# Kernel optimization log

Measured on AMD Instinct MI355X. Metric: run time of the kernel, lower is better.

## Reference

```python
import jax, jax.numpy as jnp
import numpy as np

N = 100_000      # nodes
E = 1_600_000    # edges (avg degree 16)
F = 64           # node feature dim (node_channels)
H = 64           # hidden_channels
ED = 16          # edge_embedding_size
NEG_SLOPE = 0.2


def _lin(k, fi, fo):
    return jax.random.normal(k, (fi, fo), jnp.float32) / np.sqrt(fi)


def setup_inputs() -> dict:
    key = jax.random.key(0)
    ks = jax.random.split(key, 24)
    inp = {
        "x": jax.random.normal(ks[0], (N, F), jnp.float32),
        "edge_index": jax.random.randint(ks[1], (2, E), 0, N, dtype=jnp.int64),
        "edge_attr": jax.random.normal(ks[2], (E, ED), jnp.float32),
        # conv1 (GATv2Conv -> H)
        "Wl1": _lin(ks[3], F, H), "bl1": jnp.zeros((H,), jnp.float32),
        "Wr1": _lin(ks[4], F, H), "br1": jnp.zeros((H,), jnp.float32),
        "We1": _lin(ks[5], ED, H),
        "a1": jax.random.normal(ks[6], (H,), jnp.float32) / np.sqrt(H),
        "cb1": jnp.zeros((H,), jnp.float32),
        # lin1 residual (F -> H)
        "L1w": _lin(ks[7], F, H), "L1b": jnp.zeros((H,), jnp.float32),
        # conv2 (GATv2Conv -> F)
        "Wl2": _lin(ks[8], H, F), "bl2": jnp.zeros((F,), jnp.float32),
        "Wr2": _lin(ks[9], H, F), "br2": jnp.zeros((F,), jnp.float32),
        "We2": _lin(ks[10], ED, F),
        "a2": jax.random.normal(ks[11], (F,), jnp.float32) / np.sqrt(F),
        "cb2": jnp.zeros((F,), jnp.float32),
        # lin2 residual (H -> F)
        "L2w": _lin(ks[12], H, F), "L2b": jnp.zeros((F,), jnp.float32),
    }
    return inp


def _gatv2(x, src, dst, edge_attr, Wl, bl, Wr, br, We, a, cb):
    # GATv2, heads=1, add_self_loops=False, lin_edge bias-free
    xl = x @ Wl + bl                      # [N, D] source transform (also the value)
    xr = x @ Wr + br                      # [N, D] target transform
    m = xl[src] + xr[dst] + edge_attr @ We  # [E, D]
    s = jax.nn.leaky_relu(m, NEG_SLOPE) @ a  # [E] attention logits
    smax = jax.ops.segment_max(s, dst, num_segments=N)
    ex = jnp.exp(s - smax[dst])
    den = jax.ops.segment_sum(ex, dst, num_segments=N)
    alpha = ex / (den[dst] + 1e-16)       # softmax over incoming edges per target
    out = jax.ops.segment_sum(alpha[:, None] * xl[src], dst, num_segments=N)
    return out + cb


def reference(x, edge_index, edge_attr,
              Wl1, bl1, Wr1, br1, We1, a1, cb1, L1w, L1b,
              Wl2, bl2, Wr2, br2, We2, a2, cb2, L2w, L2b):
    src, dst = edge_index[0], edge_index[1]
    h = _gatv2(x, src, dst, edge_attr, Wl1, bl1, Wr1, br1, We1, a1, cb1) + x @ L1w + L1b
    h = jax.nn.relu(h)
    out = _gatv2(h, src, dst, edge_attr, Wl2, bl2, Wr2, br2, We2, a2, cb2) + h @ L2w + L2b
    return out
```

## Files before the change

### kernel.cpp

```cpp
#include <hip/hip_runtime.h>
#include <hip/hip_fp16.h>
#include <math.h>

#define D 64
#define EDIM 16
#define NEG 0.2f
#define SCHUNK 1024

typedef _Float16 hh2 __attribute__((ext_vector_type(2)));
union H2cvt { unsigned u; hh2 v; __half2 h; };

__global__ void node_transform(const float* __restrict__ x,
                               const float* __restrict__ Wl, const float* __restrict__ bl,
                               const float* __restrict__ Wr, const float* __restrict__ br,
                               const float* __restrict__ Lw, const float* __restrict__ Lb,
                               __half* __restrict__ xlh, float* __restrict__ xr,
                               float* __restrict__ res, int N)
{
    __shared__ float wl[D * D], wr[D * D], lw[D * D];
    for (int i = threadIdx.x; i < D * D / 4; i += blockDim.x) {
        ((float4*)wl)[i] = ((const float4*)Wl)[i];
        ((float4*)wr)[i] = ((const float4*)Wr)[i];
        ((float4*)lw)[i] = ((const float4*)Lw)[i];
    }
    int lane = threadIdx.x & 63;
    int wave = __builtin_amdgcn_readfirstlane(threadIdx.x >> 6);
    float vbl = bl[lane], vbr = br[lane], vlb = Lb[lane];
    __syncthreads();

    int gwave  = blockIdx.x * 4 + wave;
    int nwaves = gridDim.x * 4;
    for (int n0 = gwave * 8; n0 < N; n0 += nwaves * 8) {
        float al[8], ar[8], ae[8];
        #pragma unroll
        for (int j = 0; j < 8; j++) { al[j] = vbl; ar[j] = vbr; ae[j] = vlb; }

        if (n0 + 8 <= N) {
            const float* xp0 = x + (size_t)n0 * D;
            #pragma unroll 4
            for (int k = 0; k < D; k++) {
                float w1 = wl[k * D + lane];
                float w2 = wr[k * D + lane];
                float w3 = lw[k * D + lane];
                #pragma unroll
                for (int j = 0; j < 8; j++) {
                    float xv = xp0[j * D + k];
                    al[j] = fmaf(xv, w1, al[j]);
                    ar[j] = fmaf(xv, w2, ar[j]);
                    ae[j] = fmaf(xv, w3, ae[j]);
                }
            }
            #pragma unroll
            for (int j = 0; j < 8; j++) {
                int n = n0 + j;
                xlh[(size_t)n * D + lane] = __float2half(al[j]);
                xr[(size_t)n * D + lane]  = ar[j];
                res[(size_t)n * D + lane] = ae[j];
            }
        } else {
            int nr = N - n0;
            for (int k = 0; k < D; k++) {
                float w1 = wl[k * D + lane];
                float w2 = wr[k * D + lane];
                float w3 = lw[k * D + lane];
                for (int j = 0; j < nr; j++) {
                    float xv = x[(size_t)(n0 + j) * D + k];
                    al[j] = fmaf(xv, w1, al[j]);
                    ar[j] = fmaf(xv, w2, ar[j]);
                    ae[j] = fmaf(xv, w3, ae[j]);
                }
            }
            for (int j = 0; j < nr; j++) {
                int n = n0 + j;
                xlh[(size_t)n * D + lane] = __float2half(al[j]);
                xr[(size_t)n * D + lane]  = ar[j];
                res[(size_t)n * D + lane] = ae[j];
            }
        }
    }
}

__global__ void count_deg(const int* __restrict__ ei, int* __restrict__ deg, int E)
{
    int e = blockIdx.x * blockDim.x + threadIdx.x;
    if (e < E) atomicAdd(&deg[ei[E + e]], 1);
}

__global__ void scan_blocks(const int* __restrict__ deg, int* __restrict__ rowptr,
                            int* __restrict__ bsum, int N)
{
    __shared__ int tsum[256];
    int t = threadIdx.x;
    int base = blockIdx.x * SCHUNK + t * 4;
    int v0 = 0, v1 = 0, v2 = 0, v3 = 0;
    if (base + 3 < N) {
        const int4 q = *(const int4*)(deg + base);
        v0 = q.x; v1 = q.y; v2 = q.z; v3 = q.w;
    } else {
        if (base + 0 < N) v0 = deg[base + 0];
        if (base + 1 < N) v1 = deg[base + 1];
        if (base + 2 < N) v2 = deg[base + 2];
        if (base + 3 < N) v3 = deg[base + 3];
    }
    int local = v0 + v1 + v2 + v3;
    tsum[t] = local;
    __syncthreads();
    for (int off = 1; off < 256; off <<= 1) {
        int x = (t >= off) ? tsum[t - off] : 0;
        __syncthreads();
        tsum[t] += x;
        __syncthreads();
    }
    int excl = tsum[t] - local;
    if (base + 0 < N) rowptr[base + 0] = excl;
    if (base + 1 < N) rowptr[base + 1] = excl + v0;
    if (base + 2 < N) rowptr[base + 2] = excl + v0 + v1;
    if (base + 3 < N) rowptr[base + 3] = excl + v0 + v1 + v2;
    if (t == 0) bsum[blockIdx.x] = tsum[255];
}

__global__ void scan_bsums(int* __restrict__ bsum, int nb, int* __restrict__ rowptrN)
{
    __shared__ int part[256];
    int t = threadIdx.x;
    int C = (nb + 255) / 256;
    int b = t * C, e = min(b + C, nb);
    int sum = 0;
    for (int i = b; i < e; i++) sum += bsum[i];
    part[t] = sum;
    __syncthreads();
    for (int off = 1; off < 256; off <<= 1) {
        int x = (t >= off) ? part[t - off] : 0;
        __syncthreads();
        part[t] += x;
        __syncthreads();
    }
    int running = part[t] - sum;
    for (int i = b; i < e; i++) {
        int v = bsum[i];
        bsum[i] = running;
        running += v;
    }
    if (t == 255) *rowptrN = part[255];
}

__global__ void add_offsets(int* __restrict__ rowptr, const int* __restrict__ bsum, int N)
{
    int i = blockIdx.x * blockDim.x + threadIdx.x;
    if (i < N) rowptr[i] += bsum[i >> 10];
}

__global__ void scatter_edges(const int* __restrict__ ei, const float* __restrict__ eattr,
                              int* __restrict__ cursor,
                              int* __restrict__ esrc, __half* __restrict__ eah, int E)
{
    int e = blockIdx.x * blockDim.x + threadIdx.x;
    if (e >= E) return;
    int dst = ei[E + e];
    int pos = atomicAdd(&cursor[dst], 1);
    esrc[pos] = ei[e];
    const float4* s4 = (const float4*)(eattr + (size_t)e * EDIM);
    float4 f0 = s4[0], f1 = s4[1], f2 = s4[2], f3 = s4[3];
    union { __half2 h[8]; uint4 q[2]; } u;
    u.h[0] = __floats2half2_rn(f0.x, f0.y); u.h[1] = __floats2half2_rn(f0.z, f0.w);
    u.h[2] = __floats2half2_rn(f1.x, f1.y); u.h[3] = __floats2half2_rn(f1.z, f1.w);
    u.h[4] = __floats2half2_rn(f2.x, f2.y); u.h[5] = __floats2half2_rn(f2.z, f2.w);
    u.h[6] = __floats2half2_rn(f3.x, f3.y); u.h[7] = __floats2half2_rn(f3.z, f3.w);
    uint4* d4 = (uint4*)(eah + (size_t)pos * EDIM);
    d4[0] = u.q[0];
    d4[1] = u.q[1];
}

__device__ __forceinline__ float bpx(float v, int addr)
{
    return __int_as_float(__builtin_amdgcn_ds_bpermute(addr, __float_as_int(v)));
}

__device__ __forceinline__ float edge_dot(const __half* __restrict__ eah, int ee,
                                          const hh2* w2)
{
    const unsigned* ea = (const unsigned*)(eah + (size_t)ee * EDIM);
    float acc = 0.f;
    #pragma unroll
    for (int k = 0; k < 8; k++) {
        H2cvt c; c.u = ea[k];
#if defined(__has_builtin) && __has_builtin(__builtin_amdgcn_fdot2)
        acc = __builtin_amdgcn_fdot2(c.v, w2[k], acc, false);
#else
        acc += (float)(c.v[0] * w2[k][0]) + (float)(c.v[1] * w2[k][1]);
#endif
    }
    return acc;
}

__global__ void gat_fused(const int* __restrict__ rowptr, const int* __restrict__ esrc,
                          const __half* __restrict__ eah,
                          const float* __restrict__ We, const float* __restrict__ avec,
                          const __half* __restrict__ xlh, const float* __restrict__ xr,
                          const float* __restrict__ res, const float* __restrict__ cb,
                          float* __restrict__ out, int N, int do_relu)
{
    int wid = __builtin_amdgcn_readfirstlane(
        (int)((blockIdx.x * blockDim.x + threadIdx.x) >> 6));
    int lane = threadIdx.x & 63;
    if (wid >= N) return;

    hh2 w2[8];
    #pragma unroll
    for (int j = 0; j < 8; j++) {
        H2cvt c;
        c.h = __floats2half2_rn(We[(2 * j) * D + lane], We[(2 * j + 1) * D + lane]);
        w2[j] = c.v;
    }
    float av  = avec[lane];
    float xrv = xr[(size_t)wid * D + lane];
    int beg = __builtin_amdgcn_readfirstlane(rowptr[wid]);
    int end = __builtin_amdgcn_readfirstlane(rowptr[wid + 1]);

    const int la4 = lane << 2;
    const int A1 = la4 ^ 4,  A2 = la4 ^ 8,   A3 = la4 ^ 12;
    const int A4 = la4 ^ 16, A8 = la4 ^ 32,  A16 = la4 ^ 64, A32 = la4 ^ 128;

    float S4 = 0.f, Sr = 0.f, O = 0.f;
    int e = beg;
    for (; e + 4 <= end; e += 4) {
        float pp[4], xlv[4];
        #pragma unroll
        for (int j = 0; j < 4; j++) {
            int s = __builtin_amdgcn_readfirstlane(esrc[e + j]);
            xlv[j] = __half2float(xlh[(size_t)s * D + lane]);
            float ew = edge_dot(eah, e + j, w2);
            float m = xlv[j] + xrv + ew;
            float lr = fmaf(NEG, fminf(m, 0.f), fmaxf(m, 0.f));
            pp[j] = lr * av;
        }
        #pragma unroll
        for (int j = 0; j < 4; j++) pp[j] += bpx(pp[j], A1);
        #pragma unroll
        for (int j = 0; j < 4; j++) pp[j] += bpx(pp[j], A2);
        int c0 = lane & 1, c1 = lane & 2;
        float t0 = c0 ? pp[1] : pp[0];
        float t1 = c0 ? pp[3] : pp[2];
        float v  = c1 ? t1 : t0;
        v += bpx(v, A4); v += bpx(v, A8); v += bpx(v, A16); v += bpx(v, A32);
        float ev = __expf(v);
        S4 += ev;
        float q1 = bpx(ev, A1);
        float q2 = bpx(ev, A2);
        float q3 = bpx(ev, A3);
        float y0a = c0 ? xlv[1] : xlv[0], y0b = c0 ? xlv[3] : xlv[2];
        float y1a = c0 ? xlv[0] : xlv[1], y1b = c0 ? xlv[2] : xlv[3];
        float x_c  = c1 ? y0b : y0a;
        float x_c1 = c1 ? y1b : y1a;
        float x_c2 = c1 ? y0a : y0b;
        float x_c3 = c1 ? y1a : y1b;
        O = fmaf(ev, x_c, fmaf(q1, x_c1, fmaf(q2, x_c2, fmaf(q3, x_c3, O))));
    }
    for (; e < end; ++e) {
        int s = __builtin_amdgcn_readfirstlane(esrc[e]);
        float xlv = __half2float(xlh[(size_t)s * D + lane]);
        float ew = edge_dot(eah, e, w2);
        float m = xlv + xrv + ew;
        float lr = fmaf(NEG, fminf(m, 0.f), fmaxf(m, 0.f));
        float p = lr * av;
        p += bpx(p, A1); p += bpx(p, A2); p += bpx(p, A4);
        p += bpx(p, A8); p += bpx(p, A16); p += bpx(p, A32);
        float w = __expf(p);
        Sr += w;
        O = fmaf(w, xlv, O);
    }
    S4 += bpx(S4, A1);
    S4 += bpx(S4, A2);
    float S = S4 + Sr;

    float v = O / (S + 1e-16f) + cb[lane] + res[(size_t)wid * D + lane];
    if (do_relu) v = fmaxf(v, 0.f);
    out[(size_t)wid * D + lane] = v;
}

extern "C" void kernel_launch(void* const* d_in, const int* in_sizes, int n_in,
                              void* d_out, int out_size, void* d_ws, size_t ws_size,
                              hipStream_t stream)
{
    const float* x     = (const float*)d_in[0];
    const int*   ei    = (const int*)d_in[1];
    const float* eattr = (const float*)d_in[2];
    const float* Wl1 = (const float*)d_in[3];  const float* bl1 = (const float*)d_in[4];
    const float* Wr1 = (const float*)d_in[5];  const float* br1 = (const float*)d_in[6];
    const float* We1 = (const float*)d_in[7];  const float* a1  = (const float*)d_in[8];
    const float* cb1 = (const float*)d_in[9];
    const float* L1w = (const float*)d_in[10]; const float* L1b = (const float*)d_in[11];
    const float* Wl2 = (const float*)d_in[12]; const float* bl2 = (const float*)d_in[13];
    const float* Wr2 = (const float*)d_in[14]; const float* br2 = (const float*)d_in[15];
    const float* We2 = (const float*)d_in[16]; const float* a2  = (const float*)d_in[17];
    const float* cb2 = (const float*)d_in[18];
    const float* L2w = (const float*)d_in[19]; const float* L2b = (const float*)d_in[20];

    const int N = in_sizes[0] / D;
    const int E = in_sizes[1] / 2;
    const int NB = (N + SCHUNK - 1) / SCHUNK;

    char* wsb = (char*)d_ws;
    float*  xr   = (float*)wsb;  wsb += (size_t)N * D * sizeof(float);
    float*  res  = (float*)wsb;  wsb += (size_t)N * D * sizeof(float);
    __half* xlh  = (__half*)wsb; wsb += (size_t)N * D * sizeof(__half);
    __half* eah  = (__half*)wsb; wsb += (size_t)E * EDIM * sizeof(__half);
    int* esrc    = (int*)wsb;    wsb += (size_t)E * sizeof(int);
    int* deg     = (int*)wsb;    wsb += (size_t)N * sizeof(int);
    int* rowptr  = (int*)wsb;    wsb += (size_t)(N + 1) * sizeof(int);
    int* cursor  = (int*)wsb;    wsb += (size_t)N * sizeof(int);
    int* bsum    = (int*)wsb;    wsb += (size_t)NB * sizeof(int);

    float* out = (float*)d_out;

    const int et = (E + 255) / 256;
    const int nb = (N + 3) / 4;

    hipMemsetAsync(deg, 0, (size_t)N * sizeof(int), stream);
    count_deg<<<et, 256, 0, stream>>>(ei, deg, E);
    scan_blocks<<<NB, 256, 0, stream>>>(deg, rowptr, bsum, N);
    scan_bsums<<<1, 256, 0, stream>>>(bsum, NB, rowptr + N);
    add_offsets<<<(N + 255) / 256, 256, 0, stream>>>(rowptr, bsum, N);
    hipMemcpyAsync(cursor, rowptr, (size_t)N * sizeof(int),
                   hipMemcpyDeviceToDevice, stream);
    scatter_edges<<<et, 256, 0, stream>>>(ei, eattr, cursor, esrc, eah, E);

    node_transform<<<1024, 256, 0, stream>>>(x, Wl1, bl1, Wr1, br1, L1w, L1b,
                                             xlh, xr, res, N);
    gat_fused<<<nb, 256, 0, stream>>>(rowptr, esrc, eah, We1, a1,
                                      xlh, xr, res, cb1, out, N, 1);

    node_transform<<<1024, 256, 0, stream>>>(out, Wl2, bl2, Wr2, br2, L2w, L2b,
                                             xlh, xr, res, N);
    gat_fused<<<nb, 256, 0, stream>>>(rowptr, esrc, eah, We2, a2,
                                      xlh, xr, res, cb2, out, N, 0);
}
```

Baseline: 525.2 us.

## Split edge scatter into position pass and coalesced gather build

The CSR build is split in two. First an atomic pass records only the original edge index at each sorted position. Then a gather kernel reads edge attributes and sources by that index and writes them coalesced in destination order, replacing the scattered 32-byte writes. The cursor copy is folded into add_offsets, removing a memcpy. This costs an extra kernel launch and an indirect read of edge_attr, and it reuses the res buffer for eidx before node_transform overwrites it.

```diff
diff --git a/kernel.cpp b/kernel.cpp
--- a/kernel.cpp
+++ b/kernel.cpp
@@ -144,20 +144,33 @@
     if (t == 255) *rowptrN = part[255];
 }
 
-__global__ void add_offsets(int* __restrict__ rowptr, const int* __restrict__ bsum, int N)
+__global__ void add_offsets(int* __restrict__ rowptr, const int* __restrict__ bsum,
+                            int* __restrict__ cursor, int N)
 {
     int i = blockIdx.x * blockDim.x + threadIdx.x;
-    if (i < N) rowptr[i] += bsum[i >> 10];
-}
-
-__global__ void scatter_edges(const int* __restrict__ ei, const float* __restrict__ eattr,
-                              int* __restrict__ cursor,
-                              int* __restrict__ esrc, __half* __restrict__ eah, int E)
+    if (i < N) {
+        int v = rowptr[i] + bsum[i >> 10];
+        rowptr[i] = v;
+        cursor[i] = v;
+    }
+}
+
+__global__ void scatter_pos(const int* __restrict__ ei, int* __restrict__ cursor,
+                            int* __restrict__ eidx, int E)
 {
     int e = blockIdx.x * blockDim.x + threadIdx.x;
     if (e >= E) return;
-    int dst = ei[E + e];
-    int pos = atomicAdd(&cursor[dst], 1);
+    int pos = atomicAdd(&cursor[ei[E + e]], 1);
+    eidx[pos] = e;
+}
+
+__global__ void gather_build(const int* __restrict__ ei, const float* __restrict__ eattr,
+                             const int* __restrict__ eidx,
+                             int* __restrict__ esrc, __half* __restrict__ eah, int E)
+{
+    int pos = blockIdx.x * blockDim.x + threadIdx.x;
+    if (pos >= E) return;
+    int e = eidx[pos];
     esrc[pos] = ei[e];
     const float4* s4 = (const float4*)(eattr + (size_t)e * EDIM);
     float4 f0 = s4[0], f1 = s4[1], f2 = s4[2], f3 = s4[3];
@@ -310,6 +323,7 @@
     int* rowptr  = (int*)wsb;    wsb += (size_t)(N + 1) * sizeof(int);
     int* cursor  = (int*)wsb;    wsb += (size_t)N * sizeof(int);
     int* bsum    = (int*)wsb;    wsb += (size_t)NB * sizeof(int);
+    int* eidx    = (int*)res;
 
     float* out = (float*)d_out;
 
@@ -320,10 +334,9 @@
     count_deg<<<et, 256, 0, stream>>>(ei, deg, E);
     scan_blocks<<<NB, 256, 0, stream>>>(deg, rowptr, bsum, N);
     scan_bsums<<<1, 256, 0, stream>>>(bsum, NB, rowptr + N);
-    add_offsets<<<(N + 255) / 256, 256, 0, stream>>>(rowptr, bsum, N);
-    hipMemcpyAsync(cursor, rowptr, (size_t)N * sizeof(int),
-                   hipMemcpyDeviceToDevice, stream);
-    scatter_edges<<<et, 256, 0, stream>>>(ei, eattr, cursor, esrc, eah, E);
+    add_offsets<<<(N + 255) / 256, 256, 0, stream>>>(rowptr, bsum, cursor, N);
+    scatter_pos<<<et, 256, 0, stream>>>(ei, cursor, eidx, E);
+    gather_build<<<et, 256, 0, stream>>>(ei, eattr, eidx, esrc, eah, E);
 
     node_transform<<<1024, 256, 0, stream>>>(x, Wl1, bl1, Wr1, br1, L1w, L1b,
                                              xlh, xr, res, N);
```

New measurement: 606.2 us. +15.4%, slower.

## Pad atomic counters to 64B, fuse cursor init, unroll edge loop by eight

Applied to the files above, without the earlier changes.

Degree and cursor counters are spread out to one per 64-byte line, placed in the res buffer, so atomics on nearby nodes stop contending for the same cache line. The add_offsets kernel now writes the cursor directly, which drops the device-to-device memcpy. The gather loop gains an 8-edge unrolled path that interleaves two 4-edge groups for more memory-level parallelism. In exchange the memset now clears 16x more memory, the scan loses its vectorized loads, and the edge loop uses more registers.

```diff
diff --git a/kernel.cpp b/kernel.cpp
--- a/kernel.cpp
+++ b/kernel.cpp
@@ -6,6 +6,7 @@
 #define EDIM 16
 #define NEG 0.2f
 #define SCHUNK 1024
+#define PAD 4
 
 typedef _Float16 hh2 __attribute__((ext_vector_type(2)));
 union H2cvt { unsigned u; hh2 v; __half2 h; };
@@ -80,28 +81,23 @@
     }
 }
 
-__global__ void count_deg(const int* __restrict__ ei, int* __restrict__ deg, int E)
+__global__ void count_deg(const int* __restrict__ ei, int* __restrict__ degp, int E)
 {
     int e = blockIdx.x * blockDim.x + threadIdx.x;
-    if (e < E) atomicAdd(&deg[ei[E + e]], 1);
-}
-
-__global__ void scan_blocks(const int* __restrict__ deg, int* __restrict__ rowptr,
+    if (e < E) atomicAdd(&degp[ei[E + e] << PAD], 1);
+}
+
+__global__ void scan_blocks(const int* __restrict__ degp, int* __restrict__ rowptr,
                             int* __restrict__ bsum, int N)
 {
     __shared__ int tsum[256];
     int t = threadIdx.x;
     int base = blockIdx.x * SCHUNK + t * 4;
     int v0 = 0, v1 = 0, v2 = 0, v3 = 0;
-    if (base + 3 < N) {
-        const int4 q = *(const int4*)(deg + base);
-        v0 = q.x; v1 = q.y; v2 = q.z; v3 = q.w;
-    } else {
-        if (base + 0 < N) v0 = deg[base + 0];
-        if (base + 1 < N) v1 = deg[base + 1];
-        if (base + 2 < N) v2 = deg[base + 2];
-        if (base + 3 < N) v3 = deg[base + 3];
-    }
+    if (base + 0 < N) v0 = degp[(base + 0) << PAD];
+    if (base + 1 < N) v1 = degp[(base + 1) << PAD];
+    if (base + 2 < N) v2 = degp[(base + 2) << PAD];
+    if (base + 3 < N) v3 = degp[(base + 3) << PAD];
     int local = v0 + v1 + v2 + v3;
     tsum[t] = local;
     __syncthreads();
@@ -144,20 +140,25 @@
     if (t == 255) *rowptrN = part[255];
 }
 
-__global__ void add_offsets(int* __restrict__ rowptr, const int* __restrict__ bsum, int N)
+__global__ void add_offsets(int* __restrict__ rowptr, const int* __restrict__ bsum,
+                            int* __restrict__ cursorp, int N)
 {
     int i = blockIdx.x * blockDim.x + threadIdx.x;
-    if (i < N) rowptr[i] += bsum[i >> 10];
+    if (i < N) {
+        int v = rowptr[i] + bsum[i >> 10];
+        rowptr[i] = v;
+        cursorp[i << PAD] = v;
+    }
 }
 
 __global__ void scatter_edges(const int* __restrict__ ei, const float* __restrict__ eattr,
-                              int* __restrict__ cursor,
+                              int* __restrict__ cursorp,
                               int* __restrict__ esrc, __half* __restrict__ eah, int E)
 {
     int e = blockIdx.x * blockDim.x + threadIdx.x;
     if (e >= E) return;
     int dst = ei[E + e];
-    int pos = atomicAdd(&cursor[dst], 1);
+    int pos = atomicAdd(&cursorp[dst << PAD], 1);
     esrc[pos] = ei[e];
     const float4* s4 = (const float4*)(eattr + (size_t)e * EDIM);
     float4 f0 = s4[0], f1 = s4[1], f2 = s4[2], f3 = s4[3];
@@ -220,9 +221,54 @@
     const int la4 = lane << 2;
     const int A1 = la4 ^ 4,  A2 = la4 ^ 8,   A3 = la4 ^ 12;
     const int A4 = la4 ^ 16, A8 = la4 ^ 32,  A16 = la4 ^ 64, A32 = la4 ^ 128;
+    int c0 = lane & 1, c1 = lane & 2;
 
     float S4 = 0.f, Sr = 0.f, O = 0.f;
     int e = beg;
+    for (; e + 8 <= end; e += 8) {
+        float pA[4], xA[4], pB[4], xB[4];
+        #pragma unroll
+        for (int j = 0; j < 4; j++) {
+            int s = __builtin_amdgcn_readfirstlane(esrc[e + j]);
+            xA[j] = __half2float(xlh[(size_t)s * D + lane]);
+            float ew = edge_dot(eah, e + j, w2);
+            float m = xA[j] + xrv + ew;
+            pA[j] = fmaf(NEG, fminf(m, 0.f), fmaxf(m, 0.f)) * av;
+        }
+        #pragma unroll
+        for (int j = 0; j < 4; j++) {
+            int s = __builtin_amdgcn_readfirstlane(esrc[e + 4 + j]);
+            xB[j] = __half2float(xlh[(size_t)s * D + lane]);
+            float ew = edge_dot(eah, e + 4 + j, w2);
+            float m = xB[j] + xrv + ew;
+            pB[j] = fmaf(NEG, fminf(m, 0.f), fmaxf(m, 0.f)) * av;
+        }
+        #pragma unroll
+        for (int j = 0; j < 4; j++) { pA[j] += bpx(pA[j], A1); pB[j] += bpx(pB[j], A1); }
+        #pragma unroll
+        for (int j = 0; j < 4; j++) { pA[j] += bpx(pA[j], A2); pB[j] += bpx(pB[j], A2); }
+        float vA = c1 ? (c0 ? pA[3] : pA[2]) : (c0 ? pA[1] : pA[0]);
+        float vB = c1 ? (c0 ? pB[3] : pB[2]) : (c0 ? pB[1] : pB[0]);
+        vA += bpx(vA, A4);  vB += bpx(vB, A4);
+        vA += bpx(vA, A8);  vB += bpx(vB, A8);
+        vA += bpx(vA, A16); vB += bpx(vB, A16);
+        vA += bpx(vA, A32); vB += bpx(vB, A32);
+        float evA = __expf(vA), evB = __expf(vB);
+        S4 += evA; S4 += evB;
+        float qA1 = bpx(evA, A1), qB1 = bpx(evB, A1);
+        float qA2 = bpx(evA, A2), qB2 = bpx(evB, A2);
+        float qA3 = bpx(evA, A3), qB3 = bpx(evB, A3);
+        float y0a = c0 ? xA[1] : xA[0], y0b = c0 ? xA[3] : xA[2];
+        float y1a = c0 ? xA[0] : xA[1], y1b = c0 ? xA[2] : xA[3];
+        float xcA  = c1 ? y0b : y0a, xc1A = c1 ? y1b : y1a;
+        float xc2A = c1 ? y0a : y0b, xc3A = c1 ? y1a : y1b;
+        O = fmaf(evA, xcA, fmaf(qA1, xc1A, fmaf(qA2, xc2A, fmaf(qA3, xc3A, O))));
+        float z0a = c0 ? xB[1] : xB[0], z0b = c0 ? xB[3] : xB[2];
+        float z1a = c0 ? xB[0] : xB[1], z1b = c0 ? xB[2] : xB[3];
+        float xcB  = c1 ? z0b : z0a, xc1B = c1 ? z1b : z1a;
+        float xc2B = c1 ? z0a : z0b, xc3B = c1 ? z1a : z1b;
+        O = fmaf(evB, xcB, fmaf(qB1, xc1B, fmaf(qB2, xc2B, fmaf(qB3, xc3B, O))));
+    }
     for (; e + 4 <= end; e += 4) {
         float pp[4], xlv[4];
         #pragma unroll
@@ -231,14 +277,12 @@
             xlv[j] = __half2float(xlh[(size_t)s * D + lane]);
             float ew = edge_dot(eah, e + j, w2);
             float m = xlv[j] + xrv + ew;
-            float lr = fmaf(NEG, fminf(m, 0.f), fmaxf(m, 0.f));
-            pp[j] = lr * av;
+            pp[j] = fmaf(NEG, fminf(m, 0.f), fmaxf(m, 0.f)) * av;
         }
         #pragma unroll
         for (int j = 0; j < 4; j++) pp[j] += bpx(pp[j], A1);
         #pragma unroll
         for (int j = 0; j < 4; j++) pp[j] += bpx(pp[j], A2);
-        int c0 = lane & 1, c1 = lane & 2;
         float t0 = c0 ? pp[1] : pp[0];
         float t1 = c0 ? pp[3] : pp[2];
         float v  = c1 ? t1 : t0;
@@ -261,8 +305,7 @@
         float xlv = __half2float(xlh[(size_t)s * D + lane]);
         float ew = edge_dot(eah, e, w2);
         float m = xlv + xrv + ew;
-        float lr = fmaf(NEG, fminf(m, 0.f), fmaxf(m, 0.f));
-        float p = lr * av;
+        float p = fmaf(NEG, fminf(m, 0.f), fmaxf(m, 0.f)) * av;
         p += bpx(p, A1); p += bpx(p, A2); p += bpx(p, A4);
         p += bpx(p, A8); p += bpx(p, A16); p += bpx(p, A32);
         float w = __expf(p);
@@ -306,24 +349,22 @@
     __half* xlh  = (__half*)wsb; wsb += (size_t)N * D * sizeof(__half);
     __half* eah  = (__half*)wsb; wsb += (size_t)E * EDIM * sizeof(__half);
     int* esrc    = (int*)wsb;    wsb += (size_t)E * sizeof(int);
-    int* deg     = (int*)wsb;    wsb += (size_t)N * sizeof(int);
     int* rowptr  = (int*)wsb;    wsb += (size_t)(N + 1) * sizeof(int);
-    int* cursor  = (int*)wsb;    wsb += (size_t)N * sizeof(int);
     int* bsum    = (int*)wsb;    wsb += (size_t)NB * sizeof(int);
+    int* degp    = (int*)res;
+    int* cursorp = (int*)res + ((size_t)N << PAD);
 
     float* out = (float*)d_out;
 
     const int et = (E + 255) / 256;
     const int nb = (N + 3) / 4;
 
-    hipMemsetAsync(deg, 0, (size_t)N * sizeof(int), stream);
-    count_deg<<<et, 256, 0, stream>>>(ei, deg, E);
-    scan_blocks<<<NB, 256, 0, stream>>>(deg, rowptr, bsum, N);
+    hipMemsetAsync(degp, 0, ((size_t)N << PAD) * sizeof(int), stream);
+    count_deg<<<et, 256, 0, stream>>>(ei, degp, E);
+    scan_blocks<<<NB, 256, 0, stream>>>(degp, rowptr, bsum, N);
     scan_bsums<<<1, 256, 0, stream>>>(bsum, NB, rowptr + N);
-    add_offsets<<<(N + 255) / 256, 256, 0, stream>>>(rowptr, bsum, N);
-    hipMemcpyAsync(cursor, rowptr, (size_t)N * sizeof(int),
-                   hipMemcpyDeviceToDevice, stream);
-    scatter_edges<<<et, 256, 0, stream>>>(ei, eattr, cursor, esrc, eah, E);
+    add_offsets<<<(N + 255) / 256, 256, 0, stream>>>(rowptr, bsum, cursorp, N);
+    scatter_edges<<<et, 256, 0, stream>>>(ei, eattr, cursorp, esrc, eah, E);
 
     node_transform<<<1024, 256, 0, stream>>>(x, Wl1, bl1, Wr1, br1, L1w, L1b,
                                              xlh, xr, res, N);
```

Measured after the change: 498.4 us. 1.05x faster.
